# Kernel optimization log

Hardware: AMD Instinct MI355X
Metric: run time of the kernel (lower is better)

The kernel has to match this reference:

```python
import jax, jax.numpy as jnp
import numpy as np

HEAD_DIM = 128
NUM_BUCKETS = 32
MAX_DISTANCE = 128


def _rel_pos_bucket(seq_len):
    # T5 causal relative-position bucketing (lucidrains flash-pytorch version)
    pos = jnp.arange(seq_len)
    rel = pos[None, :] - pos[:, None]          # k_pos - q_pos
    n = jnp.maximum(-rel, 0)                   # causal: only past distances
    max_exact = NUM_BUCKETS // 2
    is_small = n < max_exact
    n_safe = jnp.maximum(n, 1).astype(jnp.float32)
    val_large = max_exact + (
        jnp.log(n_safe / max_exact) / np.log(MAX_DISTANCE / max_exact)
        * (NUM_BUCKETS - max_exact)
    ).astype(jnp.int32)
    val_large = jnp.minimum(val_large, NUM_BUCKETS - 1)
    return jnp.where(is_small, n, val_large)   # (S, S) int32


def setup_inputs() -> dict:
    key = jax.random.key(0)
    ks = jax.random.split(key, 10)
    B, S, D, I = 4, 2048, 768, 1536
    s = 0.02
    return {
        "x": jax.random.normal(ks[0], (B, S, D), jnp.float32),
        "v_W": jax.random.normal(ks[1], (D, I), jnp.float32) * s,
        "v_b": jnp.zeros((I,), jnp.float32),
        "g_W": jax.random.normal(ks[2], (D, I), jnp.float32) * s,
        "g_b": jnp.zeros((I,), jnp.float32),
        "in_W": jax.random.normal(ks[3], (D, HEAD_DIM), jnp.float32) * s,
        "in_b": jnp.zeros((HEAD_DIM,), jnp.float32),
        "q_gamma": jax.random.normal(ks[4], (HEAD_DIM,), jnp.float32) * s,
        "q_beta": jnp.zeros((HEAD_DIM,), jnp.float32),
        "k_gamma": jax.random.normal(ks[5], (HEAD_DIM,), jnp.float32) * s,
        "k_beta": jnp.zeros((HEAD_DIM,), jnp.float32),
        "out_W": jax.random.normal(ks[6], (I, D), jnp.float32) * s,
        "out_b": jnp.zeros((D,), jnp.float32),
        "rel_emb": jax.random.normal(ks[7], (NUM_BUCKETS, 1), jnp.float32) * s,
    }


def reference(x, v_W, v_b, g_W, g_b, in_W, in_b,
              q_gamma, q_beta, k_gamma, k_beta, out_W, out_b, rel_emb):
    silu = jax.nn.silu
    S = x.shape[1]
    v = silu(x @ v_W + v_b)                    # (B, S, I)
    gate = silu(x @ g_W + g_b)                 # (B, S, I)
    base = silu(x @ in_W + in_b)               # (B, S, 128)
    q = base * q_gamma + q_beta
    k = base * k_gamma + k_beta
    # scores scaled by sqrt(v dim) per torch code (v.size(-1) = inner_dim)
    attn = jnp.einsum('bns,bms->bnm', q, k) / jnp.sqrt(jnp.float32(v.shape[-1]))
    bias = rel_emb[_rel_pos_bucket(S), 0] * np.sqrt(HEAD_DIM)  # (S, S)
    attn = attn + bias
    causal = jnp.triu(jnp.ones((S, S), bool), 1)
    attn = jnp.where(causal, 0.0, attn)        # masked_fill to 0 before relu^2
    attn = jnp.square(jax.nn.relu(attn))       # ReLU^2 attention (no softmax)
    o = jnp.einsum('bnm,bme->bne', attn, v) * gate
    return o @ out_W + out_b                   # (B, S, D)
```

## Files before the change

### kernel.cpp

```cpp
#include <hip/hip_runtime.h>


typedef short short8 __attribute__((ext_vector_type(8)));
typedef float f32x4 __attribute__((ext_vector_type(4)));
typedef unsigned short us4 __attribute__((ext_vector_type(4)));
typedef float fl4 __attribute__((ext_vector_type(4)));

__device__ __forceinline__ unsigned short f2bf(float f) {
  unsigned u = __builtin_bit_cast(unsigned, f);
  u += 0x7FFFu + ((u >> 16) & 1u);
  return (unsigned short)(u >> 16);
}
__device__ __forceinline__ float bf2f(unsigned short b) {
  return __builtin_bit_cast(float, ((unsigned)b) << 16);
}
__device__ __forceinline__ float silu_f(float x) { return x / (1.0f + __expf(-x)); }

__device__ __forceinline__ void gl_lds16(const void* gp, void* lp) {
  __builtin_amdgcn_global_load_lds((const __attribute__((address_space(1))) void*)gp,
                                   (__attribute__((address_space(3))) void*)lp, 16, 0, 0);
}

template <int CALLS>
__device__ __forceinline__ void stage_sw(const unsigned short* __restrict__ g,
                                         int row_stride, int r0, int ko,
                                         unsigned short* lds, int w, int l) {
#pragma unroll
  for (int c = 0; c < CALLS; ++c) {
    int e = ((w * CALLS + c) << 9) + l * 8;
    int row = e >> 6;
    int gcol = ((((e >> 3) & 7) ^ (row & 7)) << 3);
    gl_lds16(g + (size_t)(r0 + row) * row_stride + (ko + gcol), lds + e);
  }
}
__device__ __forceinline__ void stage_sw128(const unsigned short* __restrict__ g, int r0,
                                            unsigned short* lds, int w, int l) {
#pragma unroll
  for (int c = 0; c < 8; ++c) {
    int e = ((w * 8 + c) << 9) + l * 8;
    int row = e >> 7;
    int gcol = ((((e >> 3) & 15) ^ (row & 7)) << 3);
    gl_lds16(g + (size_t)(r0 + row) * 128 + gcol, lds + e);
  }
}

__device__ __forceinline__ void mfma_sw(const unsigned short* As, const unsigned short* Bs,
                                        f32x4 acc[4][4], int wm, int wn, int quad, int lc) {
  const int x7 = lc & 7;
#pragma unroll
  for (int kk = 0; kk < 2; ++kk) {
    short8 af[4], bfr[4];
#pragma unroll
    for (int i = 0; i < 4; ++i)
      af[i] = *(const short8*)&As[(wm + i * 16 + lc) * 64 + (((kk * 4 + quad) ^ x7) << 3)];
#pragma unroll
    for (int j = 0; j < 4; ++j)
      bfr[j] = *(const short8*)&Bs[(wn + j * 16 + lc) * 64 + (((kk * 4 + quad) ^ x7) << 3)];
#pragma unroll
    for (int i = 0; i < 4; ++i)
#pragma unroll
      for (int j = 0; j < 4; ++j)
        acc[i][j] = __builtin_amdgcn_mfma_f32_16x16x32_bf16(af[i], bfr[j], acc[i][j], 0, 0, 0);
  }
}

__device__ __forceinline__ void mfma_sw256(const unsigned short* As, const unsigned short* Bs,
                                           f32x4 acc[8][4], int wm, int wn, int quad, int lc) {
  const int x7 = lc & 7;
#pragma unroll
  for (int kk = 0; kk < 2; ++kk) {
    short8 af[8], bfr[4];
#pragma unroll
    for (int i = 0; i < 8; ++i)
      af[i] = *(const short8*)&As[(wm + i * 16 + lc) * 64 + (((kk * 4 + quad) ^ x7) << 3)];
#pragma unroll
    for (int j = 0; j < 4; ++j)
      bfr[j] = *(const short8*)&Bs[(wn + j * 16 + lc) * 64 + (((kk * 4 + quad) ^ x7) << 3)];
#pragma unroll
    for (int i = 0; i < 8; ++i)
#pragma unroll
      for (int j = 0; j < 4; ++j)
        acc[i][j] = __builtin_amdgcn_mfma_f32_16x16x32_bf16(af[i], bfr[j], acc[i][j], 0, 0, 0);
  }
}

__global__ __launch_bounds__(256, 2) void g123_k(
    const unsigned short* __restrict__ X,
    const unsigned short* __restrict__ Wst,
    unsigned short* __restrict__ vt,
    unsigned short* __restrict__ gateT,
    unsigned short* __restrict__ wq,
    unsigned short* __restrict__ wk,
    const float* __restrict__ v_b, const float* __restrict__ g_b,
    const float* __restrict__ in_b, const float* __restrict__ q_g,
    const float* __restrict__ q_be, const float* __restrict__ k_g,
    const float* __restrict__ k_be) {
  __shared__ unsigned short As[256 * 64];
  __shared__ unsigned short Bs[128 * 64];
  const int t = threadIdx.x, l = t & 63, w = t >> 6;
  const int id = blockIdx.x;
  const int xcd = id & 7, rest = id >> 3;
  const int n = rest % 25, m = (rest / 25) * 8 + xcd;
  const int m0 = m * 256, n0 = n * 128;
  const int wm = (w >> 1) * 128, wn = (w & 1) * 64;
  const int quad = l >> 4, lr = quad * 4, lc = l & 15;

  f32x4 acc[8][4] = {};
  for (int ko = 0; ko < 768; ko += 64) {
    stage_sw<8>(X, 768, m0, ko, As, w, l);
    stage_sw<4>(Wst, 768, n0, ko, Bs, w, l);
    __syncthreads();
    mfma_sw256(As, Bs, acc, wm, wn, quad, lc);
    __syncthreads();
  }

#pragma unroll
  for (int i = 0; i < 8; ++i) {
    const int gm = m0 + wm + i * 16 + lr;
#pragma unroll
    for (int j = 0; j < 4; ++j) {
      const int gn = n0 + wn + j * 16 + lc;
      f32x4 a = acc[i][j];
      if (n0 < 1536) {
        float bv = v_b[gn];
        us4 pk;
#pragma unroll
        for (int r = 0; r < 4; ++r) pk[r] = f2bf(silu_f(a[r] + bv));
        size_t off = (size_t)(gm >> 11) * (1536 * 2048) + (size_t)gn * 2048 + (gm & 2047);
        *(us4*)&vt[off] = pk;
      } else if (n0 < 3072) {
        float bv = g_b[gn - 1536];
        us4 pk;
#pragma unroll
        for (int r = 0; r < 4; ++r) pk[r] = f2bf(silu_f(a[r] + bv));
        *(us4*)&gateT[(size_t)(gn - 1536) * 8192 + gm] = pk;
      } else {
        int h = gn - 3072;
        float bb = in_b[h], qg = q_g[h], qb = q_be[h], kg = k_g[h], kb = k_be[h];
#pragma unroll
        for (int r = 0; r < 4; ++r) {
          float s = silu_f(a[r] + bb);
          wq[(size_t)(gm + r) * 128 + h] = f2bf(s * qg + qb);
          wk[(size_t)(gm + r) * 128 + h] = f2bf(s * kg + kb);
        }
      }
    }
  }
}

__global__ __launch_bounds__(256) void scores_k(
    const unsigned short* __restrict__ wk, const unsigned short* __restrict__ wq,
    unsigned short* __restrict__ P, const float* __restrict__ btab) {
  __shared__ unsigned short As[128 * 128];
  __shared__ unsigned short Bs[128 * 128];
  const int t = threadIdx.x, l = t & 63, w = t >> 6;
  const int z = blockIdx.z;
  int ti = blockIdx.x;
  int r = (int)((sqrtf((float)(8 * ti + 1)) - 1.0f) * 0.5f);
  if ((r + 1) * (r + 2) / 2 <= ti) ++r;
  int c = ti - r * (r + 1) / 2;
  const int m0 = c * 128, n0 = r * 128;
  const unsigned short* A = wk + (size_t)z * 2048 * 128;
  const unsigned short* Bt = wq + (size_t)z * 2048 * 128;
  unsigned short* Pz = P + (size_t)z * 2048 * 2048;
  const int wm = (w >> 1) * 64, wn = (w & 1) * 64;
  const int quad = l >> 4, lr = quad * 4, lc = l & 15;
  const int x7 = lc & 7;

  stage_sw128(A, m0, As, w, l);
  stage_sw128(Bt, n0, Bs, w, l);
  __syncthreads();

  f32x4 acc[4][4] = {};
#pragma unroll
  for (int kk = 0; kk < 4; ++kk) {
    short8 af[4], bfr[4];
#pragma unroll
    for (int i = 0; i < 4; ++i)
      af[i] = *(const short8*)&As[(wm + i * 16 + lc) * 128 + (((kk * 4 + quad) ^ x7) << 3)];
#pragma unroll
    for (int j = 0; j < 4; ++j)
      bfr[j] = *(const short8*)&Bs[(wn + j * 16 + lc) * 128 + (((kk * 4 + quad) ^ x7) << 3)];
#pragma unroll
    for (int i = 0; i < 4; ++i)
#pragma unroll
      for (int j = 0; j < 4; ++j)
        acc[i][j] = __builtin_amdgcn_mfma_f32_16x16x32_bf16(af[i], bfr[j], acc[i][j], 0, 0, 0);
  }

  const float SCALE = 0.025515518153991442f;
#pragma unroll
  for (int i = 0; i < 4; ++i) {
    const int gm = m0 + wm + i * 16 + lr;
#pragma unroll
    for (int j = 0; j < 4; ++j) {
      const int gn = n0 + wn + j * 16 + lc;
      us4 pk;
#pragma unroll
      for (int r2 = 0; r2 < 4; ++r2) {
        int mm = gm + r2;
        float v = 0.0f;
        if (mm <= gn) {
          float tt = fmaf(acc[i][j][r2], SCALE, btab[gn - mm]);
          tt = fmaxf(tt, 0.0f);
          v = tt * tt;
        }
        pk[r2] = f2bf(v);
      }
      *(us4*)&Pz[(size_t)gn * 2048 + gm] = pk;
    }
  }
}

__global__ __launch_bounds__(256) void og_k(
    const unsigned short* __restrict__ Vt,
    const unsigned short* __restrict__ P,
    const unsigned short* __restrict__ gateT,
    unsigned short* __restrict__ og) {
  __shared__ unsigned short As[128 * 64];
  __shared__ unsigned short Bs[128 * 64];
  const int t = threadIdx.x, l = t & 63, w = t >> 6;
  const int id = blockIdx.x;
  const int bblk = id / 96, rr = id % 96;
  const int xcd = rr & 7, mi = rr >> 3;
  const int half = xcd >> 2, z = xcd & 3;
  const int nt = 15 - 2 * bblk - (half ^ (bblk & 1));
  const int m0 = mi * 128;
  const int n0 = nt * 128;
  const int kend = n0 + 128;
  const unsigned short* A = Vt + (size_t)z * 1536 * 2048;
  const unsigned short* B = P + (size_t)z * 2048 * 2048;
  const int wm = (w >> 1) * 64, wn = (w & 1) * 64;
  const int quad = l >> 4, lr = quad * 4, lc = l & 15;

  f32x4 acc[4][4] = {};
  for (int ko = 0; ko < kend; ko += 64) {
    stage_sw<4>(A, 2048, m0, ko, As, w, l);
    stage_sw<4>(B, 2048, n0, ko, Bs, w, l);
    __syncthreads();
    mfma_sw(As, Bs, acc, wm, wn, quad, lc);
    __syncthreads();
  }
#pragma unroll
  for (int i = 0; i < 4; ++i) {
    const int gm = m0 + wm + i * 16 + lr;
#pragma unroll
    for (int j = 0; j < 4; ++j) {
      const int gn = n0 + wn + j * 16 + lc;
      us4 pk;
#pragma unroll
      for (int r2 = 0; r2 < 4; ++r2) {
        float g = bf2f(gateT[(size_t)(gm + r2) * 8192 + z * 2048 + gn]);
        pk[r2] = f2bf(acc[i][j][r2] * g);
      }
      *(us4*)&og[((size_t)z * 2048 + gn) * 1536 + gm] = pk;
    }
  }
}

__global__ __launch_bounds__(256) void gout_k(
    const unsigned short* __restrict__ A,
    const unsigned short* __restrict__ Bt,
    float* __restrict__ out, const float* __restrict__ o_b) {
  __shared__ unsigned short As[64 * 64];
  __shared__ unsigned short Bs[128 * 64];
  const int t = threadIdx.x, l = t & 63, w = t >> 6;
  const int id = blockIdx.x;
  const int xcd = id & 7, rest = id >> 3;
  const int m = rest % 12, ng = rest / 12;
  const int m0 = m * 64, n0 = (ng * 8 + xcd) * 128;
  const int wm = (w >> 1) * 32, wn = (w & 1) * 64;
  const int quad = l >> 4, lr = quad * 4, lc = l & 15;
  const int x7 = lc & 7;

  f32x4 acc[2][4] = {};
  for (int ko = 0; ko < 1536; ko += 64) {
    stage_sw<2>(A, 1536, m0, ko, As, w, l);
    stage_sw<4>(Bt, 1536, n0, ko, Bs, w, l);
    __syncthreads();
#pragma unroll
    for (int kk = 0; kk < 2; ++kk) {
      short8 af[2], bfr[4];
#pragma unroll
      for (int i = 0; i < 2; ++i)
        af[i] = *(const short8*)&As[(wm + i * 16 + lc) * 64 + (((kk * 4 + quad) ^ x7) << 3)];
#pragma unroll
      for (int j = 0; j < 4; ++j)
        bfr[j] = *(const short8*)&Bs[(wn + j * 16 + lc) * 64 + (((kk * 4 + quad) ^ x7) << 3)];
#pragma unroll
      for (int i = 0; i < 2; ++i)
#pragma unroll
        for (int j = 0; j < 4; ++j)
          acc[i][j] = __builtin_amdgcn_mfma_f32_16x16x32_bf16(af[i], bfr[j], acc[i][j], 0, 0, 0);
    }
    __syncthreads();
  }
#pragma unroll
  for (int i = 0; i < 2; ++i) {
    const int gm = m0 + wm + i * 16 + lr;
#pragma unroll
    for (int j = 0; j < 4; ++j) {
      const int gn = n0 + wn + j * 16 + lc;
      fl4 ob = *(const fl4*)&o_b[gm];
      fl4 res;
#pragma unroll
      for (int r2 = 0; r2 < 4; ++r2) res[r2] = acc[i][j][r2] + ob[r2];
      *(fl4*)&out[(size_t)gn * 768 + gm] = res;
    }
  }
}

__global__ void cvt_bf16(const float* __restrict__ in, unsigned short* __restrict__ out, int n) {
  int i = (blockIdx.x * blockDim.x + threadIdx.x) * 4;
  if (i < n) {
    fl4 v = *(const fl4*)&in[i];
    us4 o;
#pragma unroll
    for (int r = 0; r < 4; ++r) o[r] = f2bf(v[r]);
    *(us4*)&out[i] = o;
  }
}

__global__ void transpose_cvt4(const float* __restrict__ s0, unsigned short* __restrict__ d0,
                               const float* __restrict__ s1, unsigned short* __restrict__ d1,
                               const float* __restrict__ s2, unsigned short* __restrict__ d2,
                               const float* __restrict__ s3, unsigned short* __restrict__ d3,
                               const float* __restrict__ rel_emb, float* __restrict__ tab) {
  if (blockIdx.z == 4) {
    if (blockIdx.x == 0 && blockIdx.y == 0) {
      int d = threadIdx.y * 32 + threadIdx.x;
#pragma unroll
      for (int rep = 0; rep < 8; ++rep, d += 256) {
        int bucket;
        if (d < 16) {
          bucket = d;
        } else {
          float n = (float)d;
          int vl = 16 + (int)((logf(n * 0.0625f) / logf(8.0f)) * 16.0f);
          bucket = vl < 31 ? vl : 31;
        }
        tab[d] = rel_emb[bucket] * 11.3137085f;
      }
    }
    return;
  }
  __shared__ float tile[32][33];
  const float* in;
  unsigned short* out;
  int K_, N_, bxm, bym;
  switch (blockIdx.z) {
    case 0: in = s0; out = d0; K_ = 768; N_ = 1536; bxm = 48; bym = 24; break;
    case 1: in = s1; out = d1; K_ = 768; N_ = 1536; bxm = 48; bym = 24; break;
    case 2: in = s2; out = d2; K_ = 768; N_ = 128;  bxm = 4;  bym = 24; break;
    default: in = s3; out = d3; K_ = 1536; N_ = 768; bxm = 24; bym = 48; break;
  }
  if ((int)blockIdx.x >= bxm || (int)blockIdx.y >= bym) return;
  int bn = blockIdx.x * 32, bk = blockIdx.y * 32;
  int tx = threadIdx.x, ty = threadIdx.y;
#pragma unroll
  for (int i2 = 0; i2 < 32; i2 += 8)
    tile[ty + i2][tx] = in[(size_t)(bk + ty + i2) * N_ + (bn + tx)];
  __syncthreads();
#pragma unroll
  for (int i2 = 0; i2 < 32; i2 += 8)
    out[(size_t)(bn + ty + i2) * K_ + (bk + tx)] = f2bf(tile[tx][ty + i2]);
}

extern "C" void kernel_launch(void* const* d_in, const int* in_sizes, int n_in,
                              void* d_out, int out_size, void* d_ws, size_t ws_size,
                              hipStream_t stream) {
  const float* x    = (const float*)d_in[0];
  const float* vW   = (const float*)d_in[1];
  const float* v_b  = (const float*)d_in[2];
  const float* gW   = (const float*)d_in[3];
  const float* g_b  = (const float*)d_in[4];
  const float* inW  = (const float*)d_in[5];
  const float* in_b = (const float*)d_in[6];
  const float* q_g  = (const float*)d_in[7];
  const float* q_be = (const float*)d_in[8];
  const float* k_g  = (const float*)d_in[9];
  const float* k_be = (const float*)d_in[10];
  const float* oW   = (const float*)d_in[11];
  const float* o_b  = (const float*)d_in[12];
  const float* rel  = (const float*)d_in[13];

  char* p = (char*)d_ws;
  auto alloc = [&](size_t bytes) -> char* {
    char* r = p;
    p += (bytes + 255) & ~(size_t)255;
    return r;
  };
  unsigned short* x_bf   = (unsigned short*)alloc(8192ull * 768 * 2);
  unsigned short* wstack = (unsigned short*)alloc(3200ull * 768 * 2);
  unsigned short* vWt  = wstack;
  unsigned short* gWt  = wstack + 1536ull * 768;
  unsigned short* inWt = wstack + 3072ull * 768;
  unsigned short* oWt  = (unsigned short*)alloc(768ull * 1536 * 2);
  unsigned short* wq   = (unsigned short*)alloc(8192ull * 128 * 2);
  unsigned short* wk   = (unsigned short*)alloc(8192ull * 128 * 2);
  unsigned short* vt   = (unsigned short*)alloc(4ull * 1536 * 2048 * 2);
  unsigned short* gateT= (unsigned short*)alloc(1536ull * 8192 * 2);
  unsigned short* P    = (unsigned short*)alloc(4ull * 2048 * 2048 * 2);
  unsigned short* og   = (unsigned short*)alloc(8192ull * 1536 * 2);
  float* btab          = (float*)alloc(2048 * 4);

  cvt_bf16<<<dim3(6144), dim3(256), 0, stream>>>(x, x_bf, 8192 * 768);
  transpose_cvt4<<<dim3(48, 48, 5), dim3(32, 8), 0, stream>>>(vW, vWt, gW, gWt, inW, inWt,
                                                              oW, oWt, rel, btab);

  g123_k<<<dim3(800), 256, 0, stream>>>(x_bf, wstack, vt, gateT, wq, wk,
                                        v_b, g_b, in_b, q_g, q_be, k_g, k_be);
  scores_k<<<dim3(136, 1, 4), 256, 0, stream>>>(wk, wq, P, btab);
  og_k<<<dim3(768), 256, 0, stream>>>(vt, P, gateT, og);
  gout_k<<<dim3(768), 256, 0, stream>>>(oWt, og, (float*)d_out, o_b);
}
```

Measured before the change: 291.3 us.

## Prefetch next K-tile into registers to overlap global loads with MFMA

Replaces the direct global-to-LDS loads in three GEMM kernels (projection, attention-times-V, output) with a register-staged software pipeline. The next K-tile is loaded into registers while the current tile's MFMAs run, then written to LDS at the top of the next iteration. This is meant to hide global memory latency behind compute. In exchange it costs extra VGPRs, which may lower occupancy, especially in the 256-row kernel holding 12 prefetch registers alongside 32 accumulators, and it adds explicit LDS store instructions.

```diff
diff --git a/kernel.cpp b/kernel.cpp
--- a/kernel.cpp
+++ b/kernel.cpp
@@ -22,15 +22,23 @@
 }
 
 template <int CALLS>
-__device__ __forceinline__ void stage_sw(const unsigned short* __restrict__ g,
-                                         int row_stride, int r0, int ko,
-                                         unsigned short* lds, int w, int l) {
+__device__ __forceinline__ void pf_load(const unsigned short* __restrict__ g,
+                                        int row_stride, int r0, int ko,
+                                        fl4* regs, int w, int l) {
 #pragma unroll
   for (int c = 0; c < CALLS; ++c) {
     int e = ((w * CALLS + c) << 9) + l * 8;
     int row = e >> 6;
     int gcol = ((((e >> 3) & 7) ^ (row & 7)) << 3);
-    gl_lds16(g + (size_t)(r0 + row) * row_stride + (ko + gcol), lds + e);
+    regs[c] = *(const fl4*)(g + (size_t)(r0 + row) * row_stride + (ko + gcol));
+  }
+}
+template <int CALLS>
+__device__ __forceinline__ void pf_store(const fl4* regs, unsigned short* lds, int w, int l) {
+#pragma unroll
+  for (int c = 0; c < CALLS; ++c) {
+    int e = ((w * CALLS + c) << 9) + l * 8;
+    *(fl4*)(lds + e) = regs[c];
   }
 }
 __device__ __forceinline__ void stage_sw128(const unsigned short* __restrict__ g, int r0,
@@ -105,11 +113,18 @@
   const int wm = (w >> 1) * 128, wn = (w & 1) * 64;
   const int quad = l >> 4, lr = quad * 4, lc = l & 15;
 
+  fl4 pa[8], pb[4];
+  pf_load<8>(X, 768, m0, 0, pa, w, l);
+  pf_load<4>(Wst, 768, n0, 0, pb, w, l);
   f32x4 acc[8][4] = {};
-  for (int ko = 0; ko < 768; ko += 64) {
-    stage_sw<8>(X, 768, m0, ko, As, w, l);
-    stage_sw<4>(Wst, 768, n0, ko, Bs, w, l);
-    __syncthreads();
+  for (int tt = 0; tt < 12; ++tt) {
+    pf_store<8>(pa, As, w, l);
+    pf_store<4>(pb, Bs, w, l);
+    __syncthreads();
+    if (tt < 11) {
+      pf_load<8>(X, 768, m0, (tt + 1) * 64, pa, w, l);
+      pf_load<4>(Wst, 768, n0, (tt + 1) * 64, pb, w, l);
+    }
     mfma_sw256(As, Bs, acc, wm, wn, quad, lc);
     __syncthreads();
   }
@@ -227,17 +242,24 @@
   const int nt = 15 - 2 * bblk - (half ^ (bblk & 1));
   const int m0 = mi * 128;
   const int n0 = nt * 128;
-  const int kend = n0 + 128;
+  const int T = (n0 + 128) >> 6;
   const unsigned short* A = Vt + (size_t)z * 1536 * 2048;
   const unsigned short* B = P + (size_t)z * 2048 * 2048;
   const int wm = (w >> 1) * 64, wn = (w & 1) * 64;
   const int quad = l >> 4, lr = quad * 4, lc = l & 15;
 
+  fl4 pa[4], pb[4];
+  pf_load<4>(A, 2048, m0, 0, pa, w, l);
+  pf_load<4>(B, 2048, n0, 0, pb, w, l);
   f32x4 acc[4][4] = {};
-  for (int ko = 0; ko < kend; ko += 64) {
-    stage_sw<4>(A, 2048, m0, ko, As, w, l);
-    stage_sw<4>(B, 2048, n0, ko, Bs, w, l);
-    __syncthreads();
+  for (int tt = 0; tt < T; ++tt) {
+    pf_store<4>(pa, As, w, l);
+    pf_store<4>(pb, Bs, w, l);
+    __syncthreads();
+    if (tt + 1 < T) {
+      pf_load<4>(A, 2048, m0, (tt + 1) * 64, pa, w, l);
+      pf_load<4>(B, 2048, n0, (tt + 1) * 64, pb, w, l);
+    }
     mfma_sw(As, Bs, acc, wm, wn, quad, lc);
     __syncthreads();
   }
@@ -273,11 +295,18 @@
   const int quad = l >> 4, lr = quad * 4, lc = l & 15;
   const int x7 = lc & 7;
 
+  fl4 pa[2], pb[4];
+  pf_load<2>(A, 1536, m0, 0, pa, w, l);
+  pf_load<4>(Bt, 1536, n0, 0, pb, w, l);
   f32x4 acc[2][4] = {};
-  for (int ko = 0; ko < 1536; ko += 64) {
-    stage_sw<2>(A, 1536, m0, ko, As, w, l);
-    stage_sw<4>(Bt, 1536, n0, ko, Bs, w, l);
-    __syncthreads();
+  for (int tt = 0; tt < 24; ++tt) {
+    pf_store<2>(pa, As, w, l);
+    pf_store<4>(pb, Bs, w, l);
+    __syncthreads();
+    if (tt < 23) {
+      pf_load<2>(A, 1536, m0, (tt + 1) * 64, pa, w, l);
+      pf_load<4>(Bt, 1536, n0, (tt + 1) * 64, pb, w, l);
+    }
 #pragma unroll
     for (int kk = 0; kk < 2; ++kk) {
       short8 af[2], bfr[4];
```

Result: no change. 296.0 us (+1.6%).

## Split-K the output projection with larger tiles and a separate reduce kernel

Applied to the files above, without the earlier changes.

The output GEMM now uses 128x128 tiles instead of 64x128 and splits the K dimension into two halves. This keeps the grid at 768 blocks while giving each block more MFMA reuse per LDS load. Each half writes fp32 partials into reused scratch buffers (vt and P), and a new elementwise kernel adds the two partials and the bias. The cost is an extra kernel launch plus a write and re-read of two 8192x768 fp32 buffers.

```diff
diff --git a/kernel.cpp b/kernel.cpp
--- a/kernel.cpp
+++ b/kernel.cpp
@@ -261,53 +261,52 @@
 __global__ __launch_bounds__(256) void gout_k(
     const unsigned short* __restrict__ A,
     const unsigned short* __restrict__ Bt,
-    float* __restrict__ out, const float* __restrict__ o_b) {
-  __shared__ unsigned short As[64 * 64];
+    float* __restrict__ p0, float* __restrict__ p1) {
+  __shared__ unsigned short As[128 * 64];
   __shared__ unsigned short Bs[128 * 64];
   const int t = threadIdx.x, l = t & 63, w = t >> 6;
   const int id = blockIdx.x;
   const int xcd = id & 7, rest = id >> 3;
-  const int m = rest % 12, ng = rest / 12;
-  const int m0 = m * 64, n0 = (ng * 8 + xcd) * 128;
-  const int wm = (w >> 1) * 32, wn = (w & 1) * 64;
+  const int kpart = rest & 1, r2_ = rest >> 1;
+  const int m = r2_ % 6, ng = r2_ / 6;
+  const int m0 = m * 128, n0 = (ng * 8 + xcd) * 128;
+  const int kbase = kpart * 768;
+  float* out = kpart ? p1 : p0;
+  const int wm = (w >> 1) * 64, wn = (w & 1) * 64;
   const int quad = l >> 4, lr = quad * 4, lc = l & 15;
-  const int x7 = lc & 7;
-
-  f32x4 acc[2][4] = {};
-  for (int ko = 0; ko < 1536; ko += 64) {
-    stage_sw<2>(A, 1536, m0, ko, As, w, l);
-    stage_sw<4>(Bt, 1536, n0, ko, Bs, w, l);
-    __syncthreads();
-#pragma unroll
-    for (int kk = 0; kk < 2; ++kk) {
-      short8 af[2], bfr[4];
-#pragma unroll
-      for (int i = 0; i < 2; ++i)
-        af[i] = *(const short8*)&As[(wm + i * 16 + lc) * 64 + (((kk * 4 + quad) ^ x7) << 3)];
-#pragma unroll
-      for (int j = 0; j < 4; ++j)
-        bfr[j] = *(const short8*)&Bs[(wn + j * 16 + lc) * 64 + (((kk * 4 + quad) ^ x7) << 3)];
-#pragma unroll
-      for (int i = 0; i < 2; ++i)
-#pragma unroll
-        for (int j = 0; j < 4; ++j)
-          acc[i][j] = __builtin_amdgcn_mfma_f32_16x16x32_bf16(af[i], bfr[j], acc[i][j], 0, 0, 0);
-    }
-    __syncthreads();
-  }
-#pragma unroll
-  for (int i = 0; i < 2; ++i) {
+
+  f32x4 acc[4][4] = {};
+  for (int ko = 0; ko < 768; ko += 64) {
+    stage_sw<4>(A, 1536, m0, kbase + ko, As, w, l);
+    stage_sw<4>(Bt, 1536, n0, kbase + ko, Bs, w, l);
+    __syncthreads();
+    mfma_sw(As, Bs, acc, wm, wn, quad, lc);
+    __syncthreads();
+  }
+#pragma unroll
+  for (int i = 0; i < 4; ++i) {
     const int gm = m0 + wm + i * 16 + lr;
 #pragma unroll
     for (int j = 0; j < 4; ++j) {
       const int gn = n0 + wn + j * 16 + lc;
-      fl4 ob = *(const fl4*)&o_b[gm];
       fl4 res;
 #pragma unroll
-      for (int r2 = 0; r2 < 4; ++r2) res[r2] = acc[i][j][r2] + ob[r2];
+      for (int r3 = 0; r3 < 4; ++r3) res[r3] = acc[i][j][r3];
       *(fl4*)&out[(size_t)gn * 768 + gm] = res;
     }
   }
+}
+
+__global__ void reduce_out(const float* __restrict__ p0, const float* __restrict__ p1,
+                           const float* __restrict__ o_b, float* __restrict__ out) {
+  int i4 = (blockIdx.x * blockDim.x + threadIdx.x) * 4;
+  fl4 a = *(const fl4*)&p0[i4];
+  fl4 b = *(const fl4*)&p1[i4];
+  fl4 ob = *(const fl4*)&o_b[i4 % 768];
+  fl4 res;
+#pragma unroll
+  for (int r = 0; r < 4; ++r) res[r] = a[r] + b[r] + ob[r];
+  *(fl4*)&out[i4] = res;
 }
 
 __global__ void cvt_bf16(const float* __restrict__ in, unsigned short* __restrict__ out, int n) {
@@ -403,6 +402,8 @@
   unsigned short* P    = (unsigned short*)alloc(4ull * 2048 * 2048 * 2);
   unsigned short* og   = (unsigned short*)alloc(8192ull * 1536 * 2);
   float* btab          = (float*)alloc(2048 * 4);
+  float* part0 = (float*)vt;
+  float* part1 = (float*)P;
 
   cvt_bf16<<<dim3(6144), dim3(256), 0, stream>>>(x, x_bf, 8192 * 768);
   transpose_cvt4<<<dim3(48, 48, 5), dim3(32, 8), 0, stream>>>(vW, vWt, gW, gWt, inW, inWt,
@@ -412,5 +413,6 @@
                                         v_b, g_b, in_b, q_g, q_be, k_g, k_be);
   scores_k<<<dim3(136, 1, 4), 256, 0, stream>>>(wk, wq, P, btab);
   og_k<<<dim3(768), 256, 0, stream>>>(vt, P, gateT, og);
-  gout_k<<<dim3(768), 256, 0, stream>>>(oWt, og, (float*)d_out, o_b);
-}
+  gout_k<<<dim3(768), 256, 0, stream>>>(oWt, og, part0, part1);
+  reduce_out<<<dim3(6144), 256, 0, stream>>>(part0, part1, o_b, (float*)d_out);
+}
```

New measurement: 306.9 us. 1.05x slower.
